# Kernel tuning notes

Hardware: AMD Instinct MI355X
Metric: run time of the kernel (lower is better)

The kernel has to match this reference:

```python
import jax, jax.numpy as jnp
import numpy as np

C, T, D = 32, 768, 100      # n_countries, n_times, n_ages (=n_features)
H = 5                        # attention heads (EncoderLayer default)
HID_GCN = 60                 # GCN hidden features
FFN = 64                     # feed_forward_dim
NPRED = 10                   # n_predictions
LHID = 200                   # hid_linear_part_dim
NL = 3                       # encoder layers


def setup_inputs() -> dict:
    key = jax.random.key(0)
    ks = jax.random.split(key, 24)
    s = 0.05
    rn = lambda k, shp: jax.random.normal(k, shp, jnp.float32) * s
    return {
        "X": jax.random.normal(ks[0], (C, T, D), jnp.float32),
        "A": jax.random.uniform(ks[1], (C, C), jnp.float32),
        # GCN params
        "gcn_w1": rn(ks[2], (D, HID_GCN)),
        "gcn_b1": rn(ks[3], (HID_GCN,)),
        "gcn_w2": rn(ks[4], (HID_GCN, D)),
        "gcn_b2": rn(ks[5], (D,)),
        # 3 stacked encoder layers
        "enc_wq": rn(ks[6], (NL, H, D, D)),
        "enc_wk": rn(ks[7], (NL, H, D, D)),
        "enc_wv": rn(ks[8], (NL, H, D, D)),
        "enc_wm": rn(ks[9], (NL, H * D, D)),
        "enc_f1w": rn(ks[10], (NL, D, FFN)),
        "enc_f1b": rn(ks[11], (NL, FFN)),
        "enc_f2w": rn(ks[12], (NL, FFN, D)),
        "enc_f2b": rn(ks[13], (NL, D)),
        "enc_ln1g": jnp.ones((NL, D), jnp.float32),
        "enc_ln1b": jnp.zeros((NL, D), jnp.float32),
        "enc_ln2g": jnp.ones((NL, D), jnp.float32),
        "enc_ln2b": jnp.zeros((NL, D), jnp.float32),
        "lin1_w": rn(ks[14], (D, LHID)),
        "lin1_b": rn(ks[15], (LHID,)),
        "lin2_w": rn(ks[16], (LHID, D)),
        "lin2_b": rn(ks[17], (D,)),
    }


def _layer_norm(x, g, b, eps=1e-5):
    m = x.mean(-1, keepdims=True)
    v = ((x - m) ** 2).mean(-1, keepdims=True)
    return (x - m) / jnp.sqrt(v + eps) * g + b


def _encoder_layer(x, wq, wk, wv, wm, f1w, f1b, f2w, f2b, g1, b1, g2, b2):
    # x: [C, T, D]; wq/wk/wv: [H, D, D]
    Q = jnp.einsum('ctd,hde->chte', x, wq)
    K = jnp.einsum('ctd,hde->chte', x, wk)
    V = jnp.einsum('ctd,hde->chte', x, wv)
    scores = jnp.einsum('chte,chse->chts', Q, K) / jnp.sqrt(jnp.float32(D))
    attn = jax.nn.softmax(scores, axis=-1)
    out = jnp.einsum('chts,chse->chte', attn, V)        # [C,H,T,D]
    out = out.transpose(0, 2, 1, 3).reshape(x.shape[0], x.shape[1], H * D)
    x = _layer_norm(x + out @ wm, g1, b1)
    ffn = jax.nn.relu(x @ f1w + f1b) @ f2w + f2b
    return _layer_norm(x + ffn, g2, b2)


def reference(X, A, gcn_w1, gcn_b1, gcn_w2, gcn_b2,
              enc_wq, enc_wk, enc_wv, enc_wm,
              enc_f1w, enc_f1b, enc_f2w, enc_f2b,
              enc_ln1g, enc_ln1b, enc_ln2g, enc_ln2b,
              lin1_w, lin1_b, lin2_w, lin2_b):
    n = A.shape[0]
    adj = A + jnp.eye(n, dtype=A.dtype)
    adj_hat = adj / adj.sum(-1, keepdims=True)
    # GCN layer 1
    h = jnp.einsum('ij,jta->ita', adj_hat, X)
    h = jnp.einsum('ita,ao->ito', h, gcn_w1) + gcn_b1
    h = jax.nn.relu(h)
    # GCN layer 2
    h = jnp.einsum('ij,jta->ita', adj_hat, h)
    h = jnp.einsum('ita,ao->ito', h, gcn_w2) + gcn_b2
    # 3 encoder layers (fixed structural loop)
    for l in range(NL):
        h = _encoder_layer(h, enc_wq[l], enc_wk[l], enc_wv[l], enc_wm[l],
                           enc_f1w[l], enc_f1b[l], enc_f2w[l], enc_f2b[l],
                           enc_ln1g[l], enc_ln1b[l], enc_ln2g[l], enc_ln2b[l])
    last = h[:, -1, :]  # [C, D]
    def step(carry, _):
        p = (carry @ lin1_w + lin1_b) @ lin2_w + lin2_b
        return p, p
    _, preds = jax.lax.scan(step, last, None, length=NPRED)  # [NPRED, C, D]
    return preds.transpose(1, 0, 2)  # [C, NPRED, D]
```

## Files before the change

kernel.cpp:

```cpp
#include <hip/hip_runtime.h>


#define ROWS 24576

#define OFF_ADJ   0L
#define OFF_X0    1024L
#define OFF_X1    (OFF_X0 + 2457600L)
#define OFF_XROW  (OFF_X1 + 3932160L)
#define OFF_XT    (OFF_XROW + 1572864L)
#define OFF_WBF   (OFF_XT + 1572864L)
#define OFF_MHT   (OFF_WBF + 6291456L)
#define OFF_USTT  (OFF_MHT + 122880L)
#define OFF_MP    (OFF_USTT + 98304L)
#define OFF_C0    (OFF_MP + 10000L)
#define OFF_F1WT  (OFF_C0 + 128L)
#define OFF_F2WT  (OFF_F1WT + 12288L)
#define OFF_GW1T  (OFF_F2WT + 10752L)
#define OFF_GW2T  (OFF_GW1T + 4096L)

typedef __attribute__((ext_vector_type(8))) short short8;
typedef __attribute__((ext_vector_type(4))) float float4v;
typedef __attribute__((ext_vector_type(2))) unsigned int uint2v;

__device__ inline unsigned short f2bf(float f) {
    unsigned u = __builtin_bit_cast(unsigned, f);
    return (unsigned short)((u + 0x7fffu + ((u >> 16) & 1u)) >> 16);
}
__device__ inline unsigned pk2bf(float lo, float hi) {
    unsigned r;
    asm("v_cvt_pk_bf16_f32 %0, %1, %2" : "=v"(r) : "v"(lo), "v"(hi));
    return r;
}
__device__ inline float bf2f(unsigned short v) {
    return __builtin_bit_cast(float, ((unsigned)v) << 16);
}
__device__ inline void gload16(const short* g, short* l) {
    __builtin_amdgcn_global_load_lds((const __attribute__((address_space(1))) void*)g,
                                     (__attribute__((address_space(3))) void*)l, 16, 0, 0);
}

__global__ void __launch_bounds__(256) k_mu2(const float* __restrict__ wq, const float* __restrict__ wk,
                                             const float* __restrict__ wv, const float* __restrict__ wm,
                                             const float* __restrict__ l1w, const float* __restrict__ l1b,
                                             const float* __restrict__ l2w, const float* __restrict__ l2b,
                                             const float* __restrict__ f1w, const float* __restrict__ f2w,
                                             const float* __restrict__ A,
                                             const float* __restrict__ gw1, const float* __restrict__ gw2,
                                             unsigned short* __restrict__ MhT, unsigned short* __restrict__ UstT,
                                             float* __restrict__ Mp, float* __restrict__ c0v,
                                             unsigned short* __restrict__ f1wT, unsigned short* __restrict__ f2wT,
                                             float* __restrict__ adjh,
                                             unsigned short* __restrict__ gw1T, unsigned short* __restrict__ gw2T) {
    int bi = blockIdx.x, tid = threadIdx.x;
    if (bi < 480) {
        int mat = bi >> 4, sub = bi & 15;
        int mode = mat / 15, idx = mat % 15, l = idx / 5, h = idx % 5;
        const float* Asrc = (mode == 0 ? wq : wv) + (l*5 + h)*10000;
        const float* Bsrc = (mode == 0) ? (wk + (l*5 + h)*10000) : (wm + l*50000 + h*10000);
        int oend = sub*625 + 625;
        for (int o = sub*625 + tid; o < oend; o += 256) {
            int r = o / 100, cix = o - (o/100)*100;
            const float* arow = Asrc + r*100;
            float acc = 0.f;
            if (mode == 0) {
                const float* brow = Bsrc + cix*100;
                for (int e = 0; e < 100; ++e) acc += arow[e] * brow[e];
                MhT[(long)(l*5 + h)*16384 + cix*128 + r] = f2bf(acc * 0.1f);
            } else {
                for (int e = 0; e < 100; ++e) acc += arow[e] * Bsrc[e*100 + cix];
                UstT[(long)l*65536 + (long)cix*512 + h*100 + r] = f2bf(acc);
            }
        }
        if (sub == 0) {
            if (mode == 0) {
                unsigned short* M0 = MhT + (long)(l*5 + h)*16384;
                for (int i = tid; i < 28*128; i += 256) M0[(100 + i/128)*128 + (i%128)] = 0;
                for (int i = tid; i < 100*28; i += 256) M0[(i/28)*128 + 100 + (i%28)] = 0;
            } else if (h == 4) {
                unsigned short* U0 = UstT + (long)l*65536;
                for (int i = tid; i < 28*512; i += 256) U0[(long)(100 + i/512)*512 + (i%512)] = 0;
                for (int i = tid; i < 100*12; i += 256) U0[(long)(i/12)*512 + 500 + (i%12)] = 0;
            }
        }
    } else if (bi < 496) {
        int sub = bi - 480;
        int oend = sub*625 + 625;
        for (int o = sub*625 + tid; o < oend; o += 256) {
            int r = o / 100, cix = o - (o/100)*100;
            const float* arow = l1w + r*200;
            float acc = 0.f;
            for (int e = 0; e < 200; ++e) acc += arow[e] * l2w[e*100 + cix];
            Mp[r*100 + cix] = acc;
        }
    } else if (bi == 496) {
        if (tid < 100) {
            float acc = l2b[tid];
            for (int e = 0; e < 200; ++e) acc += l1b[e] * l2w[e*100 + tid];
            c0v[tid] = acc;
        }
    } else if (bi < 500) {
        int l = bi - 497;
        unsigned short* F1 = f1wT + (long)l*8192;
        for (int i = tid; i < 8192; i += 256) {
            int o = i >> 7, k = i & 127;
            F1[i] = (k < 100) ? f2bf(f1w[l*6400 + k*64 + o]) : (unsigned short)0;
        }
        unsigned short* F2 = f2wT + (long)l*7168;
        for (int i = tid; i < 7168; i += 256) {
            int o2 = i >> 6, k2 = i & 63;
            F2[i] = (o2 < 100) ? f2bf(f2w[l*6400 + k2*100 + o2]) : (unsigned short)0;
        }
    } else if (bi == 500) {
        __shared__ float adj[1024];
        __shared__ float rs[32];
        for (int i = tid; i < 1024; i += 256) {
            int r = i >> 5, j = i & 31;
            adj[i] = A[i] + (r == j ? 1.f : 0.f);
        }
        __syncthreads();
        if (tid < 32) {
            float s = 0.f;
            #pragma unroll
            for (int jj = 0; jj < 32; ++jj) s += adj[tid*32 + jj];
            rs[tid] = s;
        }
        __syncthreads();
        for (int i = tid; i < 1024; i += 256) adjh[i] = adj[i] / rs[i >> 5];
    } else {
        for (int i = tid; i < 8192; i += 256) {
            int o = i >> 7, k = i & 127;
            gw1T[i] = (o < 60 && k < 100) ? f2bf(gw1[k*60 + o]) : (unsigned short)0;
        }
        for (int i = tid; i < 7168; i += 256) {
            int o = i >> 6, k = i & 63;
            gw2T[i] = (o < 100 && k < 60) ? f2bf(gw2[k*100 + o]) : (unsigned short)0;
        }
    }
}

__global__ void __launch_bounds__(128) k_gw1(const float* __restrict__ X,
                                             const unsigned short* __restrict__ gw1T,
                                             unsigned short* __restrict__ g) {
    const int tid = threadIdx.x, wave = tid >> 6, lane = tid & 63;
    const int l15 = lane & 15, l4 = lane >> 4;
    const long row = (long)blockIdx.x*32 + wave*16 + l15;
    const float* xrp = X + row*100;
    float4v acc[4];
    #pragma unroll
    for (int mt = 0; mt < 4; ++mt) acc[mt] = (float4v){0,0,0,0};
    #pragma unroll
    for (int ks = 0; ks < 4; ++ks) {
        short8 b;
        #pragma unroll
        for (int e = 0; e < 8; ++e) {
            int k = ks*32 + l4*8 + e;
            b[e] = (k < 100) ? (short)f2bf(xrp[k]) : (short)0;
        }
        #pragma unroll
        for (int mt = 0; mt < 4; ++mt) {
            short8 a = *(const short8*)((const short*)gw1T + (mt*16 + l15)*128 + ks*32 + l4*8);
            acc[mt] = __builtin_amdgcn_mfma_f32_16x16x32_bf16(a, b, acc[mt], 0, 0, 0);
        }
    }
    #pragma unroll
    for (int mt = 0; mt < 4; ++mt) {
        int o0 = mt*16 + l4*4;
        *(uint2v*)(g + row*64 + o0) =
            (uint2v){pk2bf(acc[mt][0], acc[mt][1]), pk2bf(acc[mt][2], acc[mt][3])};
    }
}

__global__ void __launch_bounds__(256) k_spmmg(const float* __restrict__ adjh,
                                               const unsigned short* __restrict__ g,
                                               const float* __restrict__ b1,
                                               unsigned short* __restrict__ hid) {
    __shared__ float adj[1024];
    int tid = threadIdx.x;
    for (int i = tid; i < 1024; i += 256) adj[i] = adjh[i];
    __syncthreads();
    long p = (long)blockIdx.x*256 + tid;
    int o = (int)(p & 63);
    float acc[32];
    #pragma unroll
    for (int i = 0; i < 32; ++i) acc[i] = 0.f;
    for (int j = 0; j < 32; ++j) {
        float xv = bf2f(g[(long)j*49152 + p]);
        #pragma unroll
        for (int i = 0; i < 32; ++i) acc[i] += adj[i*32 + j] * xv;
    }
    float bias = (o < 60) ? b1[o] : 0.f;
    #pragma unroll
    for (int i = 0; i < 32; ++i) hid[(long)i*49152 + p] = f2bf(fmaxf(acc[i] + bias, 0.f));
}

__global__ void __launch_bounds__(128) k_gw2(const unsigned short* __restrict__ hid,
                                             const unsigned short* __restrict__ gw2T,
                                             unsigned short* __restrict__ h2) {
    const int tid = threadIdx.x, wave = tid >> 6, lane = tid & 63;
    const int l15 = lane & 15, l4 = lane >> 4;
    const long row = (long)blockIdx.x*32 + wave*16 + l15;
    float4v acc[7];
    #pragma unroll
    for (int mt = 0; mt < 7; ++mt) acc[mt] = (float4v){0,0,0,0};
    #pragma unroll
    for (int ks = 0; ks < 2; ++ks) {
        short8 b = *(const short8*)((const short*)hid + row*64 + ks*32 + l4*8);
        #pragma unroll
        for (int mt = 0; mt < 7; ++mt) {
            short8 a = *(const short8*)((const short*)gw2T + (mt*16 + l15)*64 + ks*32 + l4*8);
            acc[mt] = __builtin_amdgcn_mfma_f32_16x16x32_bf16(a, b, acc[mt], 0, 0, 0);
        }
    }
    #pragma unroll
    for (int mt = 0; mt < 7; ++mt) {
        int o0 = mt*16 + l4*4;
        *(uint2v*)(h2 + row*128 + o0) =
            (uint2v){pk2bf(acc[mt][0], acc[mt][1]), pk2bf(acc[mt][2], acc[mt][3])};
    }
    *(uint2v*)(h2 + row*128 + 112 + l4*4) = (uint2v){0u, 0u};
}

__global__ void __launch_bounds__(384) k_spmmx(const float* __restrict__ adjh,
                                               const unsigned short* __restrict__ h2,
                                               const float* __restrict__ b2,
                                               float* __restrict__ x0,
                                               unsigned short* __restrict__ xrow,
                                               unsigned short* __restrict__ xT) {
    __shared__ float adj[1024];
    int tid = threadIdx.x;
    for (int i = tid; i < 1024; i += 384) adj[i] = adjh[i];
    __syncthreads();
    long p = (long)blockIdx.x*384 + tid;
    int o = (int)(p & 127);
    int t = (int)(p >> 7);
    float acc[32];
    #pragma unroll
    for (int i = 0; i < 32; ++i) acc[i] = 0.f;
    for (int j = 0; j < 32; ++j) {
        float xv = bf2f(h2[(long)j*98304 + p]);
        #pragma unroll
        for (int i = 0; i < 32; ++i) acc[i] += adj[i*32 + j] * xv;
    }
    if (o < 100) {
        float bias = b2[o];
        #pragma unroll
        for (int i = 0; i < 32; ++i) {
            float v = acc[i] + bias;
            x0[((long)i*768 + t)*100 + o] = v;
            unsigned short bv = f2bf(v);
            xrow[((long)i*768 + t)*128 + o] = bv;
            xT[(long)i*98304 + (long)o*768 + t] = bv;
        }
    } else {
        #pragma unroll
        for (int i = 0; i < 32; ++i) {
            xrow[((long)i*768 + t)*128 + o] = 0;
            if (o < 112) xT[(long)i*98304 + (long)o*768 + t] = 0;
        }
    }
}

#define QP_STRIDE 136
#define PT_STRIDE 72

__global__ void __launch_bounds__(256) k_attn7(const unsigned short* __restrict__ xrow,
                                               const unsigned short* __restrict__ xT,
                                               const unsigned short* __restrict__ MhT,
                                               unsigned short* __restrict__ Wb) {
    __shared__ __align__(16) short xr[2][64 * 128];
    __shared__ __align__(16) short xt[112 * 64];
    __shared__ __align__(16) short scratch[4][2304];
    const int tid = threadIdx.x;
    const int wave = tid >> 6, lane = tid & 63;
    const int l15 = lane & 15, l4 = lane >> 4;
    const int c = blockIdx.z, h = blockIdx.y, q0 = blockIdx.x * 128;
    short* myq = scratch[wave];
    short* pt0 = scratch[wave];
    short* pt1 = scratch[wave] + 1152;

    const short* xrg = (const short*)xrow + (long)c*768*128;
    const short* xtg = (const short*)xT + (long)c*128*768;
    const int rl4 = lane >> 4, cp16 = lane & 15;
    const int rl8 = lane >> 3, cp8 = lane & 7;
    const int njt = (wave == 3) ? 2 : 4;

    #pragma unroll
    for (int j = 0; j < 4; ++j) {
        int row = wave*16 + j*4 + rl4;
        int lc = cp16 ^ (row & 7);
        gload16(xrg + (long)row*128 + lc*8, xr[0] + (wave*16 + j*4)*128);
    }

    short8 qb0[4], qb1[4];
    {
        const short* xq = (const short*)xrow + ((long)c*768 + q0 + wave*16 + l15)*128 + l4*8;
        short8 bq0[4], bq1[4];
        #pragma unroll
        for (int kk = 0; kk < 4; ++kk) {
            bq0[kk] = *(const short8*)(xq + kk*32);
            bq1[kk] = *(const short8*)(xq + 64*128 + kk*32);
        }
        const short* Mb = (const short*)MhT + (long)h*16384 + l15*128 + l4*8;
        float4v qc0[8], qc1[8];
        #pragma unroll
        for (int mt = 0; mt < 8; ++mt) { qc0[mt] = (float4v){0,0,0,0}; qc1[mt] = (float4v){0,0,0,0}; }
        #pragma unroll
        for (int mt = 0; mt < 8; ++mt) {
            #pragma unroll
            for (int kk = 0; kk < 4; ++kk) {
                short8 a = *(const short8*)(Mb + (mt*16)*128 + kk*32);
                qc0[mt] = __builtin_amdgcn_mfma_f32_16x16x32_bf16(a, bq0[kk], qc0[mt], 0, 0, 0);
                qc1[mt] = __builtin_amdgcn_mfma_f32_16x16x32_bf16(a, bq1[kk], qc1[mt], 0, 0, 0);
            }
        }
        #pragma unroll
        for (int mt = 0; mt < 8; ++mt)
            *(uint2v*)(myq + l15*QP_STRIDE + mt*16 + l4*4) =
                (uint2v){pk2bf(qc0[mt][0], qc0[mt][1]), pk2bf(qc0[mt][2], qc0[mt][3])};
        #pragma unroll
        for (int kk = 0; kk < 4; ++kk) qb0[kk] = *(const short8*)(myq + l15*QP_STRIDE + kk*32 + l4*8);
        #pragma unroll
        for (int mt = 0; mt < 8; ++mt)
            *(uint2v*)(myq + l15*QP_STRIDE + mt*16 + l4*4) =
                (uint2v){pk2bf(qc1[mt][0], qc1[mt][1]), pk2bf(qc1[mt][2], qc1[mt][3])};
        #pragma unroll
        for (int kk = 0; kk < 4; ++kk) qb1[kk] = *(const short8*)(myq + l15*QP_STRIDE + kk*32 + l4*8);
    }

    __syncthreads();

    float4v o0[7], o1[7];
    #pragma unroll
    for (int n = 0; n < 7; ++n) { o0[n] = (float4v){0,0,0,0}; o1[n] = (float4v){0,0,0,0}; }
    float lsum0 = 0.f, lsum1 = 0.f;

    for (int kt = 0; kt < 12; ++kt) {
        const int key0 = kt * 64;
        const short* xrb = xr[kt & 1];

        for (int j = 0; j < njt; ++j) {
            int row = wave*32 + j*8 + rl8;
            int lc = cp8 ^ (row & 7);
            gload16(xtg + (long)row*768 + key0 + lc*8, xt + (wave*32 + j*8)*64);
        }
        if (kt < 11) {
            short* xrn = xr[(kt + 1) & 1];
            #pragma unroll
            for (int j = 0; j < 4; ++j) {
                int row = wave*16 + j*4 + rl4;
                int lc = cp16 ^ (row & 7);
                gload16(xrg + (long)(key0 + 64 + row)*128 + lc*8, xrn + (wave*16 + j*4)*128);
            }
        }
        __builtin_amdgcn_sched_barrier(0);

        float4v s0[4], s1[4];
        #pragma unroll
        for (int kn = 0; kn < 4; ++kn) { s0[kn] = (float4v){0,0,0,0}; s1[kn] = (float4v){0,0,0,0}; }
        #pragma unroll
        for (int kn = 0; kn < 4; ++kn) {
            #pragma unroll
            for (int kk = 0; kk < 4; ++kk) {
                short8 a = *(const short8*)(xrb + (kn*16 + l15)*128 + (((kk*4 + l4) ^ (l15 & 7))*8));
                s0[kn] = __builtin_amdgcn_mfma_f32_16x16x32_bf16(a, qb0[kk], s0[kn], 0, 0, 0);
                s1[kn] = __builtin_amdgcn_mfma_f32_16x16x32_bf16(a, qb1[kk], s1[kn], 0, 0, 0);
            }
        }

        #pragma unroll
        for (int kn = 0; kn < 4; ++kn) {
            float p0[4], p1[4];
            #pragma unroll
            for (int r = 0; r < 4; ++r) {
                p0[r] = __expf(s0[kn][r]); lsum0 += p0[r];
                p1[r] = __expf(s1[kn][r]); lsum1 += p1[r];
            }
            *(uint2v*)(pt0 + l15*PT_STRIDE + kn*16 + l4*4) =
                (uint2v){pk2bf(p0[0], p0[1]), pk2bf(p0[2], p0[3])};
            *(uint2v*)(pt1 + l15*PT_STRIDE + kn*16 + l4*4) =
                (uint2v){pk2bf(p1[0], p1[1]), pk2bf(p1[2], p1[3])};
        }

        if (kt < 11) { asm volatile("s_waitcnt vmcnt(4)" ::: "memory"); }
        else         { asm volatile("s_waitcnt vmcnt(0)" ::: "memory"); }
        __builtin_amdgcn_s_barrier();

        #pragma unroll
        for (int kk2 = 0; kk2 < 2; ++kk2) {
            short8 b0 = *(const short8*)(pt0 + l15*PT_STRIDE + kk2*32 + l4*8);
            short8 b1 = *(const short8*)(pt1 + l15*PT_STRIDE + kk2*32 + l4*8);
            #pragma unroll
            for (int dt = 0; dt < 7; ++dt) {
                short8 a = *(const short8*)(xt + (dt*16 + l15)*64 + (((kk2*4 + l4) ^ (l15 & 7))*8));
                o0[dt] = __builtin_amdgcn_mfma_f32_16x16x32_bf16(a, b0, o0[dt], 0, 0, 0);
                o1[dt] = __builtin_amdgcn_mfma_f32_16x16x32_bf16(a, b1, o1[dt], 0, 0, 0);
            }
        }
        __syncthreads();
    }

    float l0 = lsum0, l1 = lsum1;
    l0 += __shfl_xor(l0, 16, 64); l0 += __shfl_xor(l0, 32, 64);
    l1 += __shfl_xor(l1, 16, 64); l1 += __shfl_xor(l1, 32, 64);
    float inv0 = 1.f / l0, inv1 = 1.f / l1;

    unsigned short* Wo0 = Wb + ((long)(c*768 + q0 + wave*16 + l15))*512 + h*100 + l4*4;
    unsigned short* Wo1 = Wo0 + 64*512;
    #pragma unroll
    for (int dt = 0; dt < 7; ++dt) {
        if (dt < 6 || l4 == 0) {
            *(uint2v*)(Wo0 + dt*16) = (uint2v){pk2bf(o0[dt][0]*inv0, o0[dt][1]*inv0),
                                               pk2bf(o0[dt][2]*inv0, o0[dt][3]*inv0)};
            *(uint2v*)(Wo1 + dt*16) = (uint2v){pk2bf(o1[dt][0]*inv1, o1[dt][1]*inv1),
                                               pk2bf(o1[dt][2]*inv1, o1[dt][3]*inv1)};
        }
    }
    if (h == 0) {
        unsigned short* Wz = Wb + ((long)c*768 + q0)*512 + 500;
        for (int i = tid; i < 1536; i += 256) Wz[(long)(i/12)*512 + (i%12)] = 0;
    }
}

template<bool EMIT>
__global__ void __launch_bounds__(128) k_tail(const unsigned short* __restrict__ Wb,
        const unsigned short* __restrict__ UstT,
        const unsigned short* __restrict__ f1wT, const unsigned short* __restrict__ f2wT,
        const float* __restrict__ f1b, const float* __restrict__ f2b,
        const float* __restrict__ g1, const float* __restrict__ b1,
        const float* __restrict__ g2, const float* __restrict__ b2,
        float* __restrict__ x, unsigned short* __restrict__ xrow, unsigned short* __restrict__ xT) {
    __shared__ __align__(16) short zS[2][16*136];
    __shared__ __align__(16) short tS[2][16*72];
    const int tid = threadIdx.x, wave = tid >> 6, lane = tid & 63;
    const int l15 = lane & 15, l4 = lane >> 4;
    const long row = (long)blockIdx.x*32 + wave*16 + l15;
    const int cc = blockIdx.x / 24;
    const int tt = (blockIdx.x % 24)*32 + wave*16 + l15;
    short* myz = zS[wave];
    short* myt = tS[wave];

    const short* Wr = (const short*)Wb + row*512 + l4*8;
    float4v o[8];
    #pragma unroll
    for (int mt = 0; mt < 8; ++mt) o[mt] = (float4v){0,0,0,0};
    for (int ks = 0; ks < 16; ++ks) {
        short8 b = *(const short8*)(Wr + ks*32);
        #pragma unroll
        for (int mt = 0; mt < 8; ++mt) {
            short8 a = *(const short8*)((const short*)UstT + (long)(mt*16 + l15)*512 + ks*32 + l4*8);
            o[mt] = __builtin_amdgcn_mfma_f32_16x16x32_bf16(a, b, o[mt], 0, 0, 0);
        }
    }

    float zv[7][4];
    float sum = 0.f;
    #pragma unroll
    for (int mt = 0; mt < 7; ++mt) {
        int f0 = mt*16 + l4*4;
        float4 xv = {0,0,0,0};
        if (f0 < 100) xv = *(const float4*)(x + row*100 + f0);
        #pragma unroll
        for (int r = 0; r < 4; ++r) {
            float z = 0.f;
            if (f0 < 100) { z = o[mt][r] + ((const float*)&xv)[r]; sum += z; }
            zv[mt][r] = z;
        }
    }
    sum += __shfl_xor(sum, 16, 64); sum += __shfl_xor(sum, 32, 64);
    float mean = sum * 0.01f;
    float vs = 0.f;
    #pragma unroll
    for (int mt = 0; mt < 7; ++mt) {
        if (mt*16 + l4*4 < 100) {
            #pragma unroll
            for (int r = 0; r < 4; ++r) { float d = zv[mt][r] - mean; vs += d*d; }
        }
    }
    vs += __shfl_xor(vs, 16, 64); vs += __shfl_xor(vs, 32, 64);
    float inv = rsqrtf(vs * 0.01f + 1e-5f);
    float x1r[7][4];
    #pragma unroll
    for (int mt = 0; mt < 7; ++mt) {
        int f0 = mt*16 + l4*4;
        float4 gv = {0,0,0,0}, bv = {0,0,0,0};
        if (f0 < 100) { gv = *(const float4*)(g1 + f0); bv = *(const float4*)(b1 + f0); }
        #pragma unroll
        for (int r = 0; r < 4; ++r)
            x1r[mt][r] = (f0 < 100) ? (zv[mt][r] - mean) * inv * ((const float*)&gv)[r] + ((const float*)&bv)[r] : 0.f;
    }

    #pragma unroll
    for (int mt = 0; mt < 8; ++mt) {
        float v0 = (mt < 7) ? x1r[mt][0] : 0.f, v1 = (mt < 7) ? x1r[mt][1] : 0.f;
        float v2 = (mt < 7) ? x1r[mt][2] : 0.f, v3 = (mt < 7) ? x1r[mt][3] : 0.f;
        *(uint2v*)(myz + l15*136 + mt*16 + l4*4) = (uint2v){pk2bf(v0, v1), pk2bf(v2, v3)};
    }

    float4v t2[4];
    #pragma unroll
    for (int m2t = 0; m2t < 4; ++m2t) t2[m2t] = (float4v){0,0,0,0};
    #pragma unroll
    for (int ks = 0; ks < 4; ++ks) {
        short8 b = *(const short8*)(myz + l15*136 + ks*32 + l4*8);
        #pragma unroll
        for (int m2t = 0; m2t < 4; ++m2t) {
            short8 a = *(const short8*)((const short*)f1wT + (m2t*16 + l15)*128 + ks*32 + l4*8);
            t2[m2t] = __builtin_amdgcn_mfma_f32_16x16x32_bf16(a, b, t2[m2t], 0, 0, 0);
        }
    }
    #pragma unroll
    for (int m2t = 0; m2t < 4; ++m2t) {
        int m20 = m2t*16 + l4*4;
        float4 bv = *(const float4*)(f1b + m20);
        float v0 = fmaxf(t2[m2t][0] + ((const float*)&bv)[0], 0.f);
        float v1 = fmaxf(t2[m2t][1] + ((const float*)&bv)[1], 0.f);
        float v2 = fmaxf(t2[m2t][2] + ((const float*)&bv)[2], 0.f);
        float v3 = fmaxf(t2[m2t][3] + ((const float*)&bv)[3], 0.f);
        *(uint2v*)(myt + l15*72 + m20) = (uint2v){pk2bf(v0, v1), pk2bf(v2, v3)};
    }

    float4v o3[7];
    #pragma unroll
    for (int m3t = 0; m3t < 7; ++m3t) o3[m3t] = (float4v){0,0,0,0};
    #pragma unroll
    for (int ks2 = 0; ks2 < 2; ++ks2) {
        short8 b = *(const short8*)(myt + l15*72 + ks2*32 + l4*8);
        #pragma unroll
        for (int m3t = 0; m3t < 7; ++m3t) {
            short8 a = *(const short8*)((const short*)f2wT + (m3t*16 + l15)*64 + ks2*32 + l4*8);
            o3[m3t] = __builtin_amdgcn_mfma_f32_16x16x32_bf16(a, b, o3[m3t], 0, 0, 0);
        }
    }

    float z2[7][4];
    float sum2 = 0.f;
    #pragma unroll
    for (int m3t = 0; m3t < 7; ++m3t) {
        int f0 = m3t*16 + l4*4;
        float4 bv = {0,0,0,0};
        if (f0 < 100) bv = *(const float4*)(f2b + f0);
        #pragma unroll
        for (int r = 0; r < 4; ++r) {
            float z = 0.f;
            if (f0 < 100) { z = o3[m3t][r] + ((const float*)&bv)[r] + x1r[m3t][r]; sum2 += z; }
            z2[m3t][r] = z;
        }
    }
    sum2 += __shfl_xor(sum2, 16, 64); sum2 += __shfl_xor(sum2, 32, 64);
    float mean2 = sum2 * 0.01f;
    float vs2 = 0.f;
    #pragma unroll
    for (int m3t = 0; m3t < 7; ++m3t) {
        if (m3t*16 + l4*4 < 100) {
            #pragma unroll
            for (int r = 0; r < 4; ++r) { float d = z2[m3t][r] - mean2; vs2 += d*d; }
        }
    }
    vs2 += __shfl_xor(vs2, 16, 64); vs2 += __shfl_xor(vs2, 32, 64);
    float inv2 = rsqrtf(vs2 * 0.01f + 1e-5f);

    unsigned short* xTc = EMIT ? (xT + (long)cc*98304 + tt) : nullptr;
    #pragma unroll
    for (int m3t = 0; m3t < 7; ++m3t) {
        int f0 = m3t*16 + l4*4;
        if (f0 < 100) {
            float4 gv = *(const float4*)(g2 + f0);
            float4 bv = *(const float4*)(b2 + f0);
            float y[4];
            #pragma unroll
            for (int r = 0; r < 4; ++r)
                y[r] = (z2[m3t][r] - mean2) * inv2 * ((const float*)&gv)[r] + ((const float*)&bv)[r];
            *(float4*)(x + row*100 + f0) = (float4){y[0], y[1], y[2], y[3]};
            if (EMIT) {
                *(uint2v*)(xrow + row*128 + f0) = (uint2v){pk2bf(y[0], y[1]), pk2bf(y[2], y[3])};
                #pragma unroll
                for (int r = 0; r < 4; ++r)
                    xTc[(long)(f0 + r)*768] = f2bf(y[r]);
            }
        } else if (EMIT) {
            *(uint2v*)(xrow + row*128 + f0) = (uint2v){0u, 0u};
            #pragma unroll
            for (int r = 0; r < 4; ++r)
                if (f0 + r < 112) xTc[(long)(f0 + r)*768] = 0;
        }
    }
    if (EMIT) *(uint2v*)(xrow + row*128 + 112 + l4*4) = (uint2v){0u, 0u};
}

__global__ void __launch_bounds__(256) k_pred2(const float* __restrict__ xf,
        const float* __restrict__ Mp, const float* __restrict__ c0v,
        float* __restrict__ out) {
    int c = blockIdx.x, tid = threadIdx.x;
    __shared__ float Ml[10000];
    __shared__ float carry[100];
    for (int i = tid; i < 10000; i += 256) Ml[i] = Mp[i];
    if (tid < 100) carry[tid] = xf[((long)c*768 + 767)*100 + tid];
    __syncthreads();
    for (int s = 0; s < 10; ++s) {
        float pv = 0.f;
        if (tid < 100) {
            pv = c0v[tid];
            for (int d = 0; d < 100; ++d) pv += carry[d] * Ml[d*100 + tid];
            out[((long)c*10 + s)*100 + tid] = pv;
        }
        __syncthreads();
        if (tid < 100) carry[tid] = pv;
        __syncthreads();
    }
}

extern "C" void kernel_launch(void* const* d_in, const int* in_sizes, int n_in,
                              void* d_out, int out_size, void* d_ws, size_t ws_size,
                              hipStream_t stream) {
    const float* X    = (const float*)d_in[0];
    const float* A    = (const float*)d_in[1];
    const float* gw1  = (const float*)d_in[2];
    const float* gb1  = (const float*)d_in[3];
    const float* gw2  = (const float*)d_in[4];
    const float* gb2  = (const float*)d_in[5];
    const float* wq   = (const float*)d_in[6];
    const float* wk   = (const float*)d_in[7];
    const float* wv   = (const float*)d_in[8];
    const float* wm   = (const float*)d_in[9];
    const float* f1w  = (const float*)d_in[10];
    const float* f1b  = (const float*)d_in[11];
    const float* f2w  = (const float*)d_in[12];
    const float* f2b  = (const float*)d_in[13];
    const float* ln1g = (const float*)d_in[14];
    const float* ln1b = (const float*)d_in[15];
    const float* ln2g = (const float*)d_in[16];
    const float* ln2b = (const float*)d_in[17];
    const float* l1w  = (const float*)d_in[18];
    const float* l1b  = (const float*)d_in[19];
    const float* l2w  = (const float*)d_in[20];
    const float* l2b  = (const float*)d_in[21];
    (void)in_sizes; (void)n_in; (void)out_size; (void)ws_size;

    float* ws   = (float*)d_ws;
    float* adjh = ws + OFF_ADJ;
    float* x0   = ws + OFF_X0;
    unsigned short* gbuf = (unsigned short*)(ws + OFF_X1);
    unsigned short* hbuf = (unsigned short*)(ws + OFF_X1 + 786432L);
    unsigned short* h2buf= (unsigned short*)(ws + OFF_X1 + 1572864L);
    unsigned short* xrow = (unsigned short*)(ws + OFF_XROW);
    unsigned short* xTb  = (unsigned short*)(ws + OFF_XT);
    unsigned short* Wbf  = (unsigned short*)(ws + OFF_WBF);
    unsigned short* MhT  = (unsigned short*)(ws + OFF_MHT);
    unsigned short* UstT = (unsigned short*)(ws + OFF_USTT);
    float* Mp   = ws + OFF_MP;
    float* c0v  = ws + OFF_C0;
    unsigned short* f1wT = (unsigned short*)(ws + OFF_F1WT);
    unsigned short* f2wT = (unsigned short*)(ws + OFF_F2WT);
    unsigned short* gw1T = (unsigned short*)(ws + OFF_GW1T);
    unsigned short* gw2T = (unsigned short*)(ws + OFF_GW2T);
    float* out  = (float*)d_out;

    k_mu2<<<502, 256, 0, stream>>>(wq, wk, wv, wm, l1w, l1b, l2w, l2b, f1w, f2w, A, gw1, gw2,
                                   MhT, UstT, Mp, c0v, f1wT, f2wT, adjh, gw1T, gw2T);

    k_gw1<<<768, 128, 0, stream>>>(X, gw1T, gbuf);
    k_spmmg<<<192, 256, 0, stream>>>(adjh, gbuf, gb1, hbuf);
    k_gw2<<<768, 128, 0, stream>>>(hbuf, gw2T, h2buf);
    k_spmmx<<<256, 384, 0, stream>>>(adjh, h2buf, gb2, x0, xrow, xTb);

    for (int l = 0; l < 3; ++l) {
        k_attn7<<<dim3(6,5,32), 256, 0, stream>>>(xrow, xTb, MhT + (long)l*81920, Wbf);
        if (l < 2)
            k_tail<true><<<768, 128, 0, stream>>>(Wbf, UstT + (long)l*65536,
                f1wT + (long)l*8192, f2wT + (long)l*7168, f1b + l*64, f2b + l*100,
                ln1g + l*100, ln1b + l*100, ln2g + l*100, ln2b + l*100, x0, xrow, xTb);
        else
            k_tail<false><<<768, 128, 0, stream>>>(Wbf, UstT + (long)l*65536,
                f1wT + (long)l*8192, f2wT + (long)l*7168, f1b + l*64, f2b + l*100,
                ln1g + l*100, ln1b + l*100, ln2g + l*100, ln2b + l*100, x0, xrow, xTb);
    }

    k_pred2<<<32, 256, 0, stream>>>(x0, Mp, c0v, out);
}
```

Baseline: 505.2 us.

## Process four query sub-tiles per wave in attention to reuse staged keys

The attention kernel now handles 256 queries per block (four 16-row sub-tiles per wave instead of two), halving the grid. Each key/value tile loaded into LDS is reused across twice as many queries, cutting global loads and LDS fills per unit of work. The probability scratch is enlarged with a new padded stride of 68, and LDS stores use short4 vector stores with compiler memory fences. In exchange, register pressure rises (28 output accumulators per wave) and only 480 blocks launch, which may hurt occupancy.

```diff
diff --git a/kernel.cpp b/kernel.cpp
--- a/kernel.cpp
+++ b/kernel.cpp
@@ -19,6 +19,7 @@
 #define OFF_GW2T  (OFF_GW1T + 4096L)
 
 typedef __attribute__((ext_vector_type(8))) short short8;
+typedef __attribute__((ext_vector_type(4))) short short4v;
 typedef __attribute__((ext_vector_type(4))) float float4v;
 typedef __attribute__((ext_vector_type(2))) unsigned int uint2v;
 
@@ -30,6 +31,9 @@
     unsigned r;
     asm("v_cvt_pk_bf16_f32 %0, %1, %2" : "=v"(r) : "v"(lo), "v"(hi));
     return r;
+}
+__device__ inline void st4s(short* p, unsigned a, unsigned b) {
+    *(short4v*)p = __builtin_bit_cast(short4v, (uint2v){a, b});
 }
 __device__ inline float bf2f(unsigned short v) {
     return __builtin_bit_cast(float, ((unsigned)v) << 16);
@@ -261,22 +265,20 @@
 }
 
 #define QP_STRIDE 136
-#define PT_STRIDE 72
-
-__global__ void __launch_bounds__(256) k_attn7(const unsigned short* __restrict__ xrow,
-                                               const unsigned short* __restrict__ xT,
-                                               const unsigned short* __restrict__ MhT,
-                                               unsigned short* __restrict__ Wb) {
+#define PT_STRIDE 68
+
+__global__ void __launch_bounds__(256) k_attn10(const unsigned short* __restrict__ xrow,
+                                                const unsigned short* __restrict__ xT,
+                                                const unsigned short* __restrict__ MhT,
+                                                unsigned short* __restrict__ Wb) {
     __shared__ __align__(16) short xr[2][64 * 128];
     __shared__ __align__(16) short xt[112 * 64];
-    __shared__ __align__(16) short scratch[4][2304];
+    __shared__ __align__(16) short scratch[4][4352];
     const int tid = threadIdx.x;
     const int wave = tid >> 6, lane = tid & 63;
     const int l15 = lane & 15, l4 = lane >> 4;
-    const int c = blockIdx.z, h = blockIdx.y, q0 = blockIdx.x * 128;
+    const int c = blockIdx.z, h = blockIdx.y, q0 = blockIdx.x * 256;
     short* myq = scratch[wave];
-    short* pt0 = scratch[wave];
-    short* pt1 = scratch[wave] + 1152;
 
     const short* xrg = (const short*)xrow + (long)c*768*128;
     const short* xtg = (const short*)xT + (long)c*128*768;
@@ -291,48 +293,47 @@
         gload16(xrg + (long)row*128 + lc*8, xr[0] + (wave*16 + j*4)*128);
     }
 
-    short8 qb0[4], qb1[4];
+    short8 qb[4][4];
     {
-        const short* xq = (const short*)xrow + ((long)c*768 + q0 + wave*16 + l15)*128 + l4*8;
-        short8 bq0[4], bq1[4];
-        #pragma unroll
-        for (int kk = 0; kk < 4; ++kk) {
-            bq0[kk] = *(const short8*)(xq + kk*32);
-            bq1[kk] = *(const short8*)(xq + 64*128 + kk*32);
-        }
         const short* Mb = (const short*)MhT + (long)h*16384 + l15*128 + l4*8;
-        float4v qc0[8], qc1[8];
-        #pragma unroll
-        for (int mt = 0; mt < 8; ++mt) { qc0[mt] = (float4v){0,0,0,0}; qc1[mt] = (float4v){0,0,0,0}; }
-        #pragma unroll
-        for (int mt = 0; mt < 8; ++mt) {
-            #pragma unroll
-            for (int kk = 0; kk < 4; ++kk) {
-                short8 a = *(const short8*)(Mb + (mt*16)*128 + kk*32);
-                qc0[mt] = __builtin_amdgcn_mfma_f32_16x16x32_bf16(a, bq0[kk], qc0[mt], 0, 0, 0);
-                qc1[mt] = __builtin_amdgcn_mfma_f32_16x16x32_bf16(a, bq1[kk], qc1[mt], 0, 0, 0);
-            }
-        }
-        #pragma unroll
-        for (int mt = 0; mt < 8; ++mt)
-            *(uint2v*)(myq + l15*QP_STRIDE + mt*16 + l4*4) =
-                (uint2v){pk2bf(qc0[mt][0], qc0[mt][1]), pk2bf(qc0[mt][2], qc0[mt][3])};
-        #pragma unroll
-        for (int kk = 0; kk < 4; ++kk) qb0[kk] = *(const short8*)(myq + l15*QP_STRIDE + kk*32 + l4*8);
-        #pragma unroll
-        for (int mt = 0; mt < 8; ++mt)
-            *(uint2v*)(myq + l15*QP_STRIDE + mt*16 + l4*4) =
-                (uint2v){pk2bf(qc1[mt][0], qc1[mt][1]), pk2bf(qc1[mt][2], qc1[mt][3])};
-        #pragma unroll
-        for (int kk = 0; kk < 4; ++kk) qb1[kk] = *(const short8*)(myq + l15*QP_STRIDE + kk*32 + l4*8);
+        #pragma unroll
+        for (int s = 0; s < 4; ++s) {
+            const short* xq = (const short*)xrow +
+                ((long)c*768 + q0 + s*64 + wave*16 + l15)*128 + l4*8;
+            short8 bq[4];
+            #pragma unroll
+            for (int kk = 0; kk < 4; ++kk) bq[kk] = *(const short8*)(xq + kk*32);
+            float4v qc[8];
+            #pragma unroll
+            for (int mt = 0; mt < 8; ++mt) qc[mt] = (float4v){0,0,0,0};
+            #pragma unroll
+            for (int mt = 0; mt < 8; ++mt) {
+                #pragma unroll
+                for (int kk = 0; kk < 4; ++kk) {
+                    short8 a = *(const short8*)(Mb + (mt*16)*128 + kk*32);
+                    qc[mt] = __builtin_amdgcn_mfma_f32_16x16x32_bf16(a, bq[kk], qc[mt], 0, 0, 0);
+                }
+            }
+            #pragma unroll
+            for (int mt = 0; mt < 8; ++mt)
+                st4s(myq + l15*QP_STRIDE + mt*16 + l4*4,
+                     pk2bf(qc[mt][0], qc[mt][1]), pk2bf(qc[mt][2], qc[mt][3]));
+            asm volatile("" ::: "memory");
+            #pragma unroll
+            for (int kk = 0; kk < 4; ++kk)
+                qb[s][kk] = *(const short8*)(myq + l15*QP_STRIDE + kk*32 + l4*8);
+            asm volatile("" ::: "memory");
+        }
     }
 
     __syncthreads();
 
-    float4v o0[7], o1[7];
-    #pragma unroll
-    for (int n = 0; n < 7; ++n) { o0[n] = (float4v){0,0,0,0}; o1[n] = (float4v){0,0,0,0}; }
-    float lsum0 = 0.f, lsum1 = 0.f;
+    float4v o[4][7];
+    #pragma unroll
+    for (int s = 0; s < 4; ++s)
+        #pragma unroll
+        for (int n = 0; n < 7; ++n) o[s][n] = (float4v){0,0,0,0};
+    float lsum[4] = {0.f, 0.f, 0.f, 0.f};
 
     for (int kt = 0; kt < 12; ++kt) {
         const int key0 = kt * 64;
@@ -354,32 +355,28 @@
         }
         __builtin_amdgcn_sched_barrier(0);
 
-        float4v s0[4], s1[4];
-        #pragma unroll
-        for (int kn = 0; kn < 4; ++kn) { s0[kn] = (float4v){0,0,0,0}; s1[kn] = (float4v){0,0,0,0}; }
         #pragma unroll
         for (int kn = 0; kn < 4; ++kn) {
+            float4v s0[4];
+            #pragma unroll
+            for (int s = 0; s < 4; ++s) s0[s] = (float4v){0,0,0,0};
             #pragma unroll
             for (int kk = 0; kk < 4; ++kk) {
                 short8 a = *(const short8*)(xrb + (kn*16 + l15)*128 + (((kk*4 + l4) ^ (l15 & 7))*8));
-                s0[kn] = __builtin_amdgcn_mfma_f32_16x16x32_bf16(a, qb0[kk], s0[kn], 0, 0, 0);
-                s1[kn] = __builtin_amdgcn_mfma_f32_16x16x32_bf16(a, qb1[kk], s1[kn], 0, 0, 0);
-            }
-        }
-
-        #pragma unroll
-        for (int kn = 0; kn < 4; ++kn) {
-            float p0[4], p1[4];
-            #pragma unroll
-            for (int r = 0; r < 4; ++r) {
-                p0[r] = __expf(s0[kn][r]); lsum0 += p0[r];
-                p1[r] = __expf(s1[kn][r]); lsum1 += p1[r];
-            }
-            *(uint2v*)(pt0 + l15*PT_STRIDE + kn*16 + l4*4) =
-                (uint2v){pk2bf(p0[0], p0[1]), pk2bf(p0[2], p0[3])};
-            *(uint2v*)(pt1 + l15*PT_STRIDE + kn*16 + l4*4) =
-                (uint2v){pk2bf(p1[0], p1[1]), pk2bf(p1[2], p1[3])};
-        }
+                #pragma unroll
+                for (int s = 0; s < 4; ++s)
+                    s0[s] = __builtin_amdgcn_mfma_f32_16x16x32_bf16(a, qb[s][kk], s0[s], 0, 0, 0);
+            }
+            #pragma unroll
+            for (int s = 0; s < 4; ++s) {
+                float p[4];
+                #pragma unroll
+                for (int r = 0; r < 4; ++r) { p[r] = __expf(s0[s][r]); lsum[s] += p[r]; }
+                st4s(scratch[wave] + s*1088 + l15*PT_STRIDE + kn*16 + l4*4,
+                     pk2bf(p[0], p[1]), pk2bf(p[2], p[3]));
+            }
+        }
+        asm volatile("" ::: "memory");
 
         if (kt < 11) { asm volatile("s_waitcnt vmcnt(4)" ::: "memory"); }
         else         { asm volatile("s_waitcnt vmcnt(0)" ::: "memory"); }
@@ -387,37 +384,38 @@
 
         #pragma unroll
         for (int kk2 = 0; kk2 < 2; ++kk2) {
-            short8 b0 = *(const short8*)(pt0 + l15*PT_STRIDE + kk2*32 + l4*8);
-            short8 b1 = *(const short8*)(pt1 + l15*PT_STRIDE + kk2*32 + l4*8);
+            short8 b[4];
+            #pragma unroll
+            for (int s = 0; s < 4; ++s)
+                b[s] = *(const short8*)(scratch[wave] + s*1088 + l15*PT_STRIDE + kk2*32 + l4*8);
             #pragma unroll
             for (int dt = 0; dt < 7; ++dt) {
                 short8 a = *(const short8*)(xt + (dt*16 + l15)*64 + (((kk2*4 + l4) ^ (l15 & 7))*8));
-                o0[dt] = __builtin_amdgcn_mfma_f32_16x16x32_bf16(a, b0, o0[dt], 0, 0, 0);
-                o1[dt] = __builtin_amdgcn_mfma_f32_16x16x32_bf16(a, b1, o1[dt], 0, 0, 0);
+                #pragma unroll
+                for (int s = 0; s < 4; ++s)
+                    o[s][dt] = __builtin_amdgcn_mfma_f32_16x16x32_bf16(a, b[s], o[s][dt], 0, 0, 0);
             }
         }
         __syncthreads();
     }
 
-    float l0 = lsum0, l1 = lsum1;
-    l0 += __shfl_xor(l0, 16, 64); l0 += __shfl_xor(l0, 32, 64);
-    l1 += __shfl_xor(l1, 16, 64); l1 += __shfl_xor(l1, 32, 64);
-    float inv0 = 1.f / l0, inv1 = 1.f / l1;
-
-    unsigned short* Wo0 = Wb + ((long)(c*768 + q0 + wave*16 + l15))*512 + h*100 + l4*4;
-    unsigned short* Wo1 = Wo0 + 64*512;
-    #pragma unroll
-    for (int dt = 0; dt < 7; ++dt) {
-        if (dt < 6 || l4 == 0) {
-            *(uint2v*)(Wo0 + dt*16) = (uint2v){pk2bf(o0[dt][0]*inv0, o0[dt][1]*inv0),
-                                               pk2bf(o0[dt][2]*inv0, o0[dt][3]*inv0)};
-            *(uint2v*)(Wo1 + dt*16) = (uint2v){pk2bf(o1[dt][0]*inv1, o1[dt][1]*inv1),
-                                               pk2bf(o1[dt][2]*inv1, o1[dt][3]*inv1)};
+    #pragma unroll
+    for (int s = 0; s < 4; ++s) {
+        float l = lsum[s];
+        l += __shfl_xor(l, 16, 64); l += __shfl_xor(l, 32, 64);
+        float inv = 1.f / l;
+        unsigned short* Wo = Wb + ((long)c*768 + q0 + s*64 + wave*16 + l15)*512 + h*100 + l4*4;
+        #pragma unroll
+        for (int dt = 0; dt < 7; ++dt) {
+            if (dt < 6 || l4 == 0) {
+                *(uint2v*)(Wo + dt*16) = (uint2v){pk2bf(o[s][dt][0]*inv, o[s][dt][1]*inv),
+                                                  pk2bf(o[s][dt][2]*inv, o[s][dt][3]*inv)};
+            }
         }
     }
     if (h == 0) {
         unsigned short* Wz = Wb + ((long)c*768 + q0)*512 + 500;
-        for (int i = tid; i < 1536; i += 256) Wz[(long)(i/12)*512 + (i%12)] = 0;
+        for (int i = tid; i < 3072; i += 256) Wz[(long)(i/12)*512 + (i%12)] = 0;
     }
 }
 
@@ -493,8 +491,9 @@
     for (int mt = 0; mt < 8; ++mt) {
         float v0 = (mt < 7) ? x1r[mt][0] : 0.f, v1 = (mt < 7) ? x1r[mt][1] : 0.f;
         float v2 = (mt < 7) ? x1r[mt][2] : 0.f, v3 = (mt < 7) ? x1r[mt][3] : 0.f;
-        *(uint2v*)(myz + l15*136 + mt*16 + l4*4) = (uint2v){pk2bf(v0, v1), pk2bf(v2, v3)};
-    }
+        st4s(myz + l15*136 + mt*16 + l4*4, pk2bf(v0, v1), pk2bf(v2, v3));
+    }
+    asm volatile("" ::: "memory");
 
     float4v t2[4];
     #pragma unroll
@@ -516,8 +515,9 @@
         float v1 = fmaxf(t2[m2t][1] + ((const float*)&bv)[1], 0.f);
         float v2 = fmaxf(t2[m2t][2] + ((const float*)&bv)[2], 0.f);
         float v3 = fmaxf(t2[m2t][3] + ((const float*)&bv)[3], 0.f);
-        *(uint2v*)(myt + l15*72 + m20) = (uint2v){pk2bf(v0, v1), pk2bf(v2, v3)};
-    }
+        st4s(myt + l15*72 + m20, pk2bf(v0, v1), pk2bf(v2, v3));
+    }
+    asm volatile("" ::: "memory");
 
     float4v o3[7];
     #pragma unroll
@@ -664,7 +664,7 @@
     k_spmmx<<<256, 384, 0, stream>>>(adjh, h2buf, gb2, x0, xrow, xTb);
 
     for (int l = 0; l < 3; ++l) {
-        k_attn7<<<dim3(6,5,32), 256, 0, stream>>>(xrow, xTb, MhT + (long)l*81920, Wbf);
+        k_attn10<<<dim3(3,5,32), 256, 0, stream>>>(xrow, xTb, MhT + (long)l*81920, Wbf);
         if (l < 2)
             k_tail<true><<<768, 128, 0, stream>>>(Wbf, UstT + (long)l*65536,
                 f1wT + (long)l*8192, f2wT + (long)l*7168, f1b + l*64, f2b + l*100,
```

After: 594.6 us. 1.18x slower.

## Keep softmax probabilities in registers and drop attention LDS scratch

Applied to the files above, without the earlier changes.

The attention kernel no longer writes exp-scores to per-wave LDS scratch and reads them back as MFMA B operands. It packs them directly into registers, using the fact that the 16x16x32 output layout matches the B layout once the V-side A operand reads are permuted into split 4-element loads. Score computation is split into two halves interleaved with the PV MFMAs. The Q-projection staging reuses the second xr buffer with an XOR swizzle, which frees the scratch array and cuts LDS use, possibly raising occupancy. In exchange, the V reads become narrower 8-byte LDS loads, and some compiler memory fences are added in the tail kernel.

```diff
diff --git a/kernel.cpp b/kernel.cpp
--- a/kernel.cpp
+++ b/kernel.cpp
@@ -19,8 +19,10 @@
 #define OFF_GW2T  (OFF_GW1T + 4096L)
 
 typedef __attribute__((ext_vector_type(8))) short short8;
+typedef __attribute__((ext_vector_type(4))) short short4v;
 typedef __attribute__((ext_vector_type(4))) float float4v;
 typedef __attribute__((ext_vector_type(2))) unsigned int uint2v;
+typedef __attribute__((ext_vector_type(4))) unsigned int uint4v;
 
 __device__ inline unsigned short f2bf(float f) {
     unsigned u = __builtin_bit_cast(unsigned, f);
@@ -30,6 +32,9 @@
     unsigned r;
     asm("v_cvt_pk_bf16_f32 %0, %1, %2" : "=v"(r) : "v"(lo), "v"(hi));
     return r;
+}
+__device__ inline void st4s(short* p, unsigned a, unsigned b) {
+    *(short4v*)p = __builtin_bit_cast(short4v, (uint2v){a, b});
 }
 __device__ inline float bf2f(unsigned short v) {
     return __builtin_bit_cast(float, ((unsigned)v) << 16);
@@ -260,29 +265,25 @@
     }
 }
 
-#define QP_STRIDE 136
-#define PT_STRIDE 72
-
-__global__ void __launch_bounds__(256) k_attn7(const unsigned short* __restrict__ xrow,
-                                               const unsigned short* __restrict__ xT,
-                                               const unsigned short* __restrict__ MhT,
-                                               unsigned short* __restrict__ Wb) {
+
+__global__ void __launch_bounds__(256) k_attn12(const unsigned short* __restrict__ xrow,
+                                                const unsigned short* __restrict__ xT,
+                                                const unsigned short* __restrict__ MhT,
+                                                unsigned short* __restrict__ Wb) {
     __shared__ __align__(16) short xr[2][64 * 128];
     __shared__ __align__(16) short xt[112 * 64];
-    __shared__ __align__(16) short scratch[4][2304];
     const int tid = threadIdx.x;
     const int wave = tid >> 6, lane = tid & 63;
     const int l15 = lane & 15, l4 = lane >> 4;
     const int c = blockIdx.z, h = blockIdx.y, q0 = blockIdx.x * 128;
-    short* myq = scratch[wave];
-    short* pt0 = scratch[wave];
-    short* pt1 = scratch[wave] + 1152;
 
     const short* xrg = (const short*)xrow + (long)c*768*128;
     const short* xtg = (const short*)xT + (long)c*128*768;
     const int rl4 = lane >> 4, cp16 = lane & 15;
     const int rl8 = lane >> 3, cp8 = lane & 7;
     const int njt = (wave == 3) ? 2 : 4;
+    const int sw8 = (l15 & 7) << 3;
+    const int swt = l15 & 7;
 
     #pragma unroll
     for (int j = 0; j < 4; ++j) {
@@ -293,6 +294,8 @@
 
     short8 qb0[4], qb1[4];
     {
+        short* mq = &xr[1][wave * 16 * 128];
+        const short* Mb = (const short*)MhT + (long)h*16384 + l15*128 + l4*8;
         const short* xq = (const short*)xrow + ((long)c*768 + q0 + wave*16 + l15)*128 + l4*8;
         short8 bq0[4], bq1[4];
         #pragma unroll
@@ -300,7 +303,6 @@
             bq0[kk] = *(const short8*)(xq + kk*32);
             bq1[kk] = *(const short8*)(xq + 64*128 + kk*32);
         }
-        const short* Mb = (const short*)MhT + (long)h*16384 + l15*128 + l4*8;
         float4v qc0[8], qc1[8];
         #pragma unroll
         for (int mt = 0; mt < 8; ++mt) { qc0[mt] = (float4v){0,0,0,0}; qc1[mt] = (float4v){0,0,0,0}; }
@@ -315,16 +317,21 @@
         }
         #pragma unroll
         for (int mt = 0; mt < 8; ++mt)
-            *(uint2v*)(myq + l15*QP_STRIDE + mt*16 + l4*4) =
-                (uint2v){pk2bf(qc0[mt][0], qc0[mt][1]), pk2bf(qc0[mt][2], qc0[mt][3])};
-        #pragma unroll
-        for (int kk = 0; kk < 4; ++kk) qb0[kk] = *(const short8*)(myq + l15*QP_STRIDE + kk*32 + l4*8);
+            st4s(mq + l15*128 + ((mt*16 + l4*4) ^ sw8),
+                 pk2bf(qc0[mt][0], qc0[mt][1]), pk2bf(qc0[mt][2], qc0[mt][3]));
+        asm volatile("" ::: "memory");
+        #pragma unroll
+        for (int kk = 0; kk < 4; ++kk)
+            qb0[kk] = *(const short8*)(mq + l15*128 + ((kk*32 + l4*8) ^ sw8));
+        asm volatile("" ::: "memory");
         #pragma unroll
         for (int mt = 0; mt < 8; ++mt)
-            *(uint2v*)(myq + l15*QP_STRIDE + mt*16 + l4*4) =
-                (uint2v){pk2bf(qc1[mt][0], qc1[mt][1]), pk2bf(qc1[mt][2], qc1[mt][3])};
-        #pragma unroll
-        for (int kk = 0; kk < 4; ++kk) qb1[kk] = *(const short8*)(myq + l15*QP_STRIDE + kk*32 + l4*8);
+            st4s(mq + l15*128 + ((mt*16 + l4*4) ^ sw8),
+                 pk2bf(qc1[mt][0], qc1[mt][1]), pk2bf(qc1[mt][2], qc1[mt][3]));
+        asm volatile("" ::: "memory");
+        #pragma unroll
+        for (int kk = 0; kk < 4; ++kk)
+            qb1[kk] = *(const short8*)(mq + l15*128 + ((kk*32 + l4*8) ^ sw8));
     }
 
     __syncthreads();
@@ -354,44 +361,76 @@
         }
         __builtin_amdgcn_sched_barrier(0);
 
-        float4v s0[4], s1[4];
-        #pragma unroll
-        for (int kn = 0; kn < 4; ++kn) { s0[kn] = (float4v){0,0,0,0}; s1[kn] = (float4v){0,0,0,0}; }
-        #pragma unroll
-        for (int kn = 0; kn < 4; ++kn) {
+        unsigned pw0[4], pw1[4];
+        #pragma unroll
+        for (int kn = 0; kn < 2; ++kn) {
+            float4v s0 = (float4v){0,0,0,0}, s1 = (float4v){0,0,0,0};
             #pragma unroll
             for (int kk = 0; kk < 4; ++kk) {
                 short8 a = *(const short8*)(xrb + (kn*16 + l15)*128 + (((kk*4 + l4) ^ (l15 & 7))*8));
-                s0[kn] = __builtin_amdgcn_mfma_f32_16x16x32_bf16(a, qb0[kk], s0[kn], 0, 0, 0);
-                s1[kn] = __builtin_amdgcn_mfma_f32_16x16x32_bf16(a, qb1[kk], s1[kn], 0, 0, 0);
-            }
-        }
-
-        #pragma unroll
-        for (int kn = 0; kn < 4; ++kn) {
+                s0 = __builtin_amdgcn_mfma_f32_16x16x32_bf16(a, qb0[kk], s0, 0, 0, 0);
+                s1 = __builtin_amdgcn_mfma_f32_16x16x32_bf16(a, qb1[kk], s1, 0, 0, 0);
+            }
             float p0[4], p1[4];
             #pragma unroll
             for (int r = 0; r < 4; ++r) {
-                p0[r] = __expf(s0[kn][r]); lsum0 += p0[r];
-                p1[r] = __expf(s1[kn][r]); lsum1 += p1[r];
-            }
-            *(uint2v*)(pt0 + l15*PT_STRIDE + kn*16 + l4*4) =
-                (uint2v){pk2bf(p0[0], p0[1]), pk2bf(p0[2], p0[3])};
-            *(uint2v*)(pt1 + l15*PT_STRIDE + kn*16 + l4*4) =
-                (uint2v){pk2bf(p1[0], p1[1]), pk2bf(p1[2], p1[3])};
+                p0[r] = __expf(s0[r]); lsum0 += p0[r];
+                p1[r] = __expf(s1[r]); lsum1 += p1[r];
+            }
+            pw0[kn*2]   = pk2bf(p0[0], p0[1]); pw0[kn*2+1] = pk2bf(p0[2], p0[3]);
+            pw1[kn*2]   = pk2bf(p1[0], p1[1]); pw1[kn*2+1] = pk2bf(p1[2], p1[3]);
         }
 
         if (kt < 11) { asm volatile("s_waitcnt vmcnt(4)" ::: "memory"); }
         else         { asm volatile("s_waitcnt vmcnt(0)" ::: "memory"); }
         __builtin_amdgcn_s_barrier();
 
-        #pragma unroll
-        for (int kk2 = 0; kk2 < 2; ++kk2) {
-            short8 b0 = *(const short8*)(pt0 + l15*PT_STRIDE + kk2*32 + l4*8);
-            short8 b1 = *(const short8*)(pt1 + l15*PT_STRIDE + kk2*32 + l4*8);
+        {
+            short8 b0 = __builtin_bit_cast(short8, (uint4v){pw0[0], pw0[1], pw0[2], pw0[3]});
+            short8 b1 = __builtin_bit_cast(short8, (uint4v){pw1[0], pw1[1], pw1[2], pw1[3]});
+            const int offLo = (((l4 >> 1) ^ swt) * 8) + (l4 & 1) * 4;
+            const int offHi = (((2 + (l4 >> 1)) ^ swt) * 8) + (l4 & 1) * 4;
             #pragma unroll
             for (int dt = 0; dt < 7; ++dt) {
-                short8 a = *(const short8*)(xt + (dt*16 + l15)*64 + (((kk2*4 + l4) ^ (l15 & 7))*8));
+                const short* xrow_t = xt + (dt*16 + l15)*64;
+                short4v lo = *(const short4v*)(xrow_t + offLo);
+                short4v hi = *(const short4v*)(xrow_t + offHi);
+                short8 a = __builtin_shufflevector(lo, hi, 0, 1, 2, 3, 4, 5, 6, 7);
+                o0[dt] = __builtin_amdgcn_mfma_f32_16x16x32_bf16(a, b0, o0[dt], 0, 0, 0);
+                o1[dt] = __builtin_amdgcn_mfma_f32_16x16x32_bf16(a, b1, o1[dt], 0, 0, 0);
+            }
+        }
+
+        #pragma unroll
+        for (int kn = 2; kn < 4; ++kn) {
+            float4v s0 = (float4v){0,0,0,0}, s1 = (float4v){0,0,0,0};
+            #pragma unroll
+            for (int kk = 0; kk < 4; ++kk) {
+                short8 a = *(const short8*)(xrb + (kn*16 + l15)*128 + (((kk*4 + l4) ^ (l15 & 7))*8));
+                s0 = __builtin_amdgcn_mfma_f32_16x16x32_bf16(a, qb0[kk], s0, 0, 0, 0);
+                s1 = __builtin_amdgcn_mfma_f32_16x16x32_bf16(a, qb1[kk], s1, 0, 0, 0);
+            }
+            float p0[4], p1[4];
+            #pragma unroll
+            for (int r = 0; r < 4; ++r) {
+                p0[r] = __expf(s0[r]); lsum0 += p0[r];
+                p1[r] = __expf(s1[r]); lsum1 += p1[r];
+            }
+            pw0[(kn-2)*2]   = pk2bf(p0[0], p0[1]); pw0[(kn-2)*2+1] = pk2bf(p0[2], p0[3]);
+            pw1[(kn-2)*2]   = pk2bf(p1[0], p1[1]); pw1[(kn-2)*2+1] = pk2bf(p1[2], p1[3]);
+        }
+
+        {
+            short8 b0 = __builtin_bit_cast(short8, (uint4v){pw0[0], pw0[1], pw0[2], pw0[3]});
+            short8 b1 = __builtin_bit_cast(short8, (uint4v){pw1[0], pw1[1], pw1[2], pw1[3]});
+            const int offLo = (((4 + (l4 >> 1)) ^ swt) * 8) + (l4 & 1) * 4;
+            const int offHi = (((6 + (l4 >> 1)) ^ swt) * 8) + (l4 & 1) * 4;
+            #pragma unroll
+            for (int dt = 0; dt < 7; ++dt) {
+                const short* xrow_t = xt + (dt*16 + l15)*64;
+                short4v lo = *(const short4v*)(xrow_t + offLo);
+                short4v hi = *(const short4v*)(xrow_t + offHi);
+                short8 a = __builtin_shufflevector(lo, hi, 0, 1, 2, 3, 4, 5, 6, 7);
                 o0[dt] = __builtin_amdgcn_mfma_f32_16x16x32_bf16(a, b0, o0[dt], 0, 0, 0);
                 o1[dt] = __builtin_amdgcn_mfma_f32_16x16x32_bf16(a, b1, o1[dt], 0, 0, 0);
             }
@@ -493,8 +532,9 @@
     for (int mt = 0; mt < 8; ++mt) {
         float v0 = (mt < 7) ? x1r[mt][0] : 0.f, v1 = (mt < 7) ? x1r[mt][1] : 0.f;
         float v2 = (mt < 7) ? x1r[mt][2] : 0.f, v3 = (mt < 7) ? x1r[mt][3] : 0.f;
-        *(uint2v*)(myz + l15*136 + mt*16 + l4*4) = (uint2v){pk2bf(v0, v1), pk2bf(v2, v3)};
-    }
+        st4s(myz + l15*136 + mt*16 + l4*4, pk2bf(v0, v1), pk2bf(v2, v3));
+    }
+    asm volatile("" ::: "memory");
 
     float4v t2[4];
     #pragma unroll
@@ -516,8 +556,9 @@
         float v1 = fmaxf(t2[m2t][1] + ((const float*)&bv)[1], 0.f);
         float v2 = fmaxf(t2[m2t][2] + ((const float*)&bv)[2], 0.f);
         float v3 = fmaxf(t2[m2t][3] + ((const float*)&bv)[3], 0.f);
-        *(uint2v*)(myt + l15*72 + m20) = (uint2v){pk2bf(v0, v1), pk2bf(v2, v3)};
-    }
+        st4s(myt + l15*72 + m20, pk2bf(v0, v1), pk2bf(v2, v3));
+    }
+    asm volatile("" ::: "memory");
 
     float4v o3[7];
     #pragma unroll
@@ -664,7 +705,7 @@
     k_spmmx<<<256, 384, 0, stream>>>(adjh, h2buf, gb2, x0, xrow, xTb);
 
     for (int l = 0; l < 3; ++l) {
-        k_attn7<<<dim3(6,5,32), 256, 0, stream>>>(xrow, xTb, MhT + (long)l*81920, Wbf);
+        k_attn12<<<dim3(6,5,32), 256, 0, stream>>>(xrow, xTb, MhT + (long)l*81920, Wbf);
         if (l < 2)
             k_tail<true><<<768, 128, 0, stream>>>(Wbf, UstT + (long)l*65536,
                 f1wT + (long)l*8192, f2wT + (long)l*7168, f1b + l*64, f2b + l*100,
```

Result: no change. 508.6 us (+0.7%).
